# Kernel tuning notes

Measured on AMD Instinct MI355X. Metric: run time of the kernel, lower is better.

Reference implementation:

```python
import jax, jax.numpy as jnp
import numpy as np

N_NODES = 100000
N_EDGES = 1600000
NODE_FEAT_DIM = 140
NUM_OPCODES = 128
EMBED_DIM = 64
HIDDEN = 128
N_LAYERS = 4
LN_EPS = 1e-5


def _layer_norm(x, g, b):
    mu = jnp.mean(x, axis=-1, keepdims=True)
    var = jnp.mean(jnp.square(x - mu), axis=-1, keepdims=True)
    return (x - mu) * jax.lax.rsqrt(var + LN_EPS) * g + b


def setup_inputs() -> dict:
    key = jax.random.key(0)
    ks = jax.random.split(key, 16)
    node_feat = jax.random.normal(ks[0], (N_NODES, NODE_FEAT_DIM), dtype=jnp.float32)
    node_opcode = jax.random.randint(ks[1], (N_NODES,), 0, NUM_OPCODES)
    topo_depth = jax.random.uniform(ks[2], (N_NODES, 1), dtype=jnp.float32)
    edge_index = jax.random.randint(ks[3], (2, N_EDGES), 0, N_NODES)
    in_dim = NODE_FEAT_DIM + EMBED_DIM + 1  # 205
    s_in = 1.0 / np.sqrt(in_dim)
    s_h = 1.0 / np.sqrt(HIDDEN)
    embed = jax.random.normal(ks[4], (NUM_OPCODES, EMBED_DIM), dtype=jnp.float32)
    embed = embed.at[0].set(0.0)  # padding_idx=0
    W_in = jax.random.uniform(ks[5], (in_dim, HIDDEN), minval=-s_in, maxval=s_in, dtype=jnp.float32)
    b_in = jax.random.uniform(ks[6], (HIDDEN,), minval=-s_in, maxval=s_in, dtype=jnp.float32)
    ln0_g = jnp.ones((HIDDEN,), jnp.float32)
    ln0_b = jnp.zeros((HIDDEN,), jnp.float32)
    # SAGEConv per layer: lin_l (neighbors, with bias), lin_r (self, no bias)
    Wl = jax.random.uniform(ks[7], (N_LAYERS, HIDDEN, HIDDEN), minval=-s_h, maxval=s_h, dtype=jnp.float32)
    bl = jax.random.uniform(ks[8], (N_LAYERS, HIDDEN), minval=-s_h, maxval=s_h, dtype=jnp.float32)
    Wr = jax.random.uniform(ks[9], (N_LAYERS, HIDDEN, HIDDEN), minval=-s_h, maxval=s_h, dtype=jnp.float32)
    ln_g = jnp.ones((N_LAYERS, HIDDEN), jnp.float32)
    ln_b = jnp.zeros((N_LAYERS, HIDDEN), jnp.float32)
    return {"node_feat": node_feat, "topo_depth": topo_depth, "embed": embed,
            "W_in": W_in, "b_in": b_in, "ln0_g": ln0_g, "ln0_b": ln0_b,
            "Wl": Wl, "bl": bl, "Wr": Wr, "ln_g": ln_g, "ln_b": ln_b,
            "node_opcode": node_opcode, "edge_index": edge_index}


def reference(node_feat, topo_depth, embed, W_in, b_in, ln0_g, ln0_b,
              Wl, bl, Wr, ln_g, ln_b, node_opcode, edge_index):
    n = node_feat.shape[0]
    op = jnp.clip(node_opcode, 0, embed.shape[0] - 1)
    h = jnp.concatenate([node_feat, embed[op], topo_depth], axis=-1)  # (n, 205)
    # input_proj: Linear -> LayerNorm -> GELU (dropout = eval identity)
    h = jax.nn.gelu(_layer_norm(h @ W_in + b_in, ln0_g, ln0_b), approximate=False)
    src, tgt = edge_index[0], edge_index[1]
    deg = jax.ops.segment_sum(jnp.ones((src.shape[0],), h.dtype), tgt, num_segments=n)
    inv_deg = (1.0 / jnp.maximum(deg, 1.0))[:, None]
    for i in range(N_LAYERS):
        # mean-SAGE: aggregate source features onto targets
        agg = jax.ops.segment_sum(h[src], tgt, num_segments=n) * inv_deg
        out = agg @ Wl[i] + bl[i] + h @ Wr[i]
        h = _layer_norm(h + jax.nn.gelu(out, approximate=False), ln_g[i], ln_b[i])
    return h
```

## Files before the change

### kernel.cpp

```cpp
#include <hip/hip_runtime.h>
#include <cstdint>
#include <cstddef>

#define NN 100000
#define NE 1600000
#define FEAT 140
#define EMB 64
#define HID 128
#define LN_EPS 1e-5f
#define BK_SHIFT 9
#define NBUCK 196
#define MAXSEG 20480

typedef unsigned int uint;
typedef unsigned short ushort;
using short8 = __attribute__((ext_vector_type(8))) short;
using f32x4  = __attribute__((ext_vector_type(4))) float;

__device__ __forceinline__ float gelu_exact(float x) {
    return 0.5f * x * (1.0f + erff(x * 0.70710678118654752440f));
}

__device__ __forceinline__ ushort f2bf(float f) {
    uint u = __float_as_uint(f);
    uint r = (u + 0x7fff + ((u >> 16) & 1)) >> 16;
    return (ushort)r;
}

__device__ __forceinline__ float bf2f(ushort u) {
    return __uint_as_float(((uint)u) << 16);
}

__device__ __forceinline__ float bflo(uint u) {
    return __uint_as_float(u << 16);
}
__device__ __forceinline__ float bfhi(uint u) {
    return __uint_as_float(u & 0xffff0000u);
}

__global__ __launch_bounds__(256) void pack_weights_kernel(
    const float* __restrict__ W_in, const float* __restrict__ Wl,
    const float* __restrict__ Wr,
    ushort* __restrict__ winp, ushort* __restrict__ wcat)
{
    const int tid = blockIdx.x * 256 + threadIdx.x;
    const int NIN = 7 * 8 * 64;
    const int NL  = 8 * 8 * 64;
    if (tid < NIN) {
        const int kk = tid >> 9;
        const int c  = (tid >> 6) & 7;
        const int l  = tid & 63;
        const int kbase = kk * 32 + (l >> 4) * 8;
        const int col = c * 16 + (l & 15);
        short8 v;
        #pragma unroll
        for (int j = 0; j < 8; ++j) {
            const int k = kbase + j;
            v[j] = (k < 205) ? (short)f2bf(W_in[k * 128 + col]) : (short)0;
        }
        *(short8*)(winp + (size_t)tid * 8) = v;
    } else if (tid < NIN + 4 * NL) {
        const int t2 = tid - NIN;
        const int layer = t2 >> 12;
        const int r = t2 & (NL - 1);
        const int kk = r >> 9;
        const int c  = (r >> 6) & 7;
        const int l  = r & 63;
        const int kbase = kk * 32 + (l >> 4) * 8;
        const int col = c * 16 + (l & 15);
        short8 v;
        #pragma unroll
        for (int j = 0; j < 8; ++j) {
            const int k = kbase + j;
            const float x = (k < 128)
                ? Wl[(size_t)layer * 16384 + k * 128 + col]
                : Wr[(size_t)layer * 16384 + (k - 128) * 128 + col];
            v[j] = (short)f2bf(x);
        }
        *(short8*)(wcat + (size_t)t2 * 8) = v;
    }
}

__global__ __launch_bounds__(256) void input_proj_mfma(
    const float* __restrict__ nf, const float* __restrict__ topo,
    const float* __restrict__ embed, const int* __restrict__ opcode,
    const ushort* __restrict__ Wp, const float* __restrict__ b_in,
    const float* __restrict__ g0, const float* __restrict__ b0,
    ushort* __restrict__ hb_out)
{
    __shared__ ushort xs[64 * 232];
    const int t = threadIdx.x;
    const int node0 = blockIdx.x * 64;

    for (int idx = t; idx < 64 * 35; idx += 256) {
        const int row = idx / 35, c = idx - row * 35;
        const int node = min(node0 + row, NN - 1);
        const float4 v = ((const float4*)nf)[(size_t)node * 35 + c];
        ushort* p = &xs[row * 232 + c * 4];
        p[0] = f2bf(v.x); p[1] = f2bf(v.y); p[2] = f2bf(v.z); p[3] = f2bf(v.w);
    }
    for (int idx = t; idx < 64 * 16; idx += 256) {
        const int row = idx >> 4, c = idx & 15;
        const int node = min(node0 + row, NN - 1);
        int op = opcode[node];
        op = min(max(op, 0), 127);
        const float4 v = ((const float4*)embed)[op * 16 + c];
        ushort* p = &xs[row * 232 + 140 + c * 4];
        p[0] = f2bf(v.x); p[1] = f2bf(v.y); p[2] = f2bf(v.z); p[3] = f2bf(v.w);
    }
    if (t < 64) {
        const int node = min(node0 + t, NN - 1);
        xs[t * 232 + 204] = f2bf(topo[node]);
    }
    for (int idx = t; idx < 64 * 19; idx += 256) {
        const int row = idx / 19, c = 205 + (idx - row * 19);
        xs[row * 232 + c] = 0;
    }
    __syncthreads();

    const int w = t >> 6, l = t & 63;
    const int gq = l >> 4, li = l & 15;

    f32x4 acc[8];
    #pragma unroll
    for (int c = 0; c < 8; ++c) acc[c] = (f32x4){0.f, 0.f, 0.f, 0.f};

    const short8* Bp = (const short8*)Wp;
    for (int kk = 0; kk < 7; ++kk) {
        const short8 a = *(const short8*)&xs[(w * 16 + li) * 232 + kk * 32 + gq * 8];
        #pragma unroll
        for (int c = 0; c < 8; ++c) {
            const short8 b = Bp[(kk * 8 + c) * 64 + l];
            acc[c] = __builtin_amdgcn_mfma_f32_16x16x32_bf16(a, b, acc[c], 0, 0, 0);
        }
    }

    float bias[8], gam[8], bet[8];
    #pragma unroll
    for (int c = 0; c < 8; ++c) {
        bias[c] = b_in[c * 16 + li];
        gam[c]  = g0[c * 16 + li];
        bet[c]  = b0[c * 16 + li];
    }
    float s[4] = {0, 0, 0, 0}, q[4] = {0, 0, 0, 0};
    #pragma unroll
    for (int c = 0; c < 8; ++c)
        #pragma unroll
        for (int r = 0; r < 4; ++r) {
            const float u = acc[c][r] + bias[c];
            acc[c][r] = u;
            s[r] += u;
            q[r] += u * u;
        }
    #pragma unroll
    for (int off = 1; off < 16; off <<= 1)
        #pragma unroll
        for (int r = 0; r < 4; ++r) {
            s[r] += __shfl_xor(s[r], off);
            q[r] += __shfl_xor(q[r], off);
        }
    #pragma unroll
    for (int r = 0; r < 4; ++r) {
        const int node = node0 + w * 16 + gq * 4 + r;
        if (node >= NN) continue;
        const float mean = s[r] * (1.0f / HID);
        const float var  = q[r] * (1.0f / HID) - mean * mean;
        const float rstd = rsqrtf(var + LN_EPS);
        #pragma unroll
        for (int c = 0; c < 8; ++c) {
            const float y = gelu_exact((acc[c][r] - mean) * rstd * gam[c] + bet[c]);
            hb_out[(size_t)node * 128 + c * 16 + li] = f2bf(y);
        }
    }
}

__global__ __launch_bounds__(256) void hist_kernel(const int* __restrict__ tgt,
                                                   int* __restrict__ bhist) {
    __shared__ int lh[NBUCK];
    for (int i = threadIdx.x; i < NBUCK; i += 256) lh[i] = 0;
    __syncthreads();
    const int e0 = blockIdx.x * 8192;
    const int eend = min(e0 + 8192, NE);
    for (int e = e0 + threadIdx.x; e < eend; e += 256)
        atomicAdd(&lh[tgt[e] >> BK_SHIFT], 1);
    __syncthreads();
    for (int i = threadIdx.x; i < NBUCK; i += 256)
        if (lh[i]) atomicAdd(&bhist[i], lh[i]);
}

__global__ __launch_bounds__(256) void bucket_scan_kernel(const int* __restrict__ bhist,
                                                          int* __restrict__ bpos,
                                                          int* __restrict__ bcur) {
    __shared__ int s_[256];
    const int t = threadIdx.x;
    int v = (t < NBUCK) ? bhist[t] : 0;
    s_[t] = v;
    __syncthreads();
    for (int off = 1; off < 256; off <<= 1) {
        int u = (t >= off) ? s_[t - off] : 0;
        __syncthreads();
        s_[t] += u;
        __syncthreads();
    }
    if (t < NBUCK) { bpos[t] = s_[t] - v; bcur[t] = s_[t] - v; }
}

__global__ __launch_bounds__(256) void partition_kernel(const int* __restrict__ src,
                                                        const int* __restrict__ tgt,
                                                        int* __restrict__ bcur,
                                                        uint2* __restrict__ pairs) {
    __shared__ int lh[NBUCK];
    __shared__ int gbase[NBUCK];
    for (int i = threadIdx.x; i < NBUCK; i += 256) lh[i] = 0;
    __syncthreads();
    const int e0 = blockIdx.x * 2048;
    const int eend = min(e0 + 2048, NE);
    int myb[8], myr[8], mys[8], myt[8];
    int cnt = 0;
    for (int e = e0 + threadIdx.x; e < eend; e += 256) {
        const int tv = tgt[e];
        const int b = tv >> BK_SHIFT;
        myb[cnt] = b; myt[cnt] = tv; mys[cnt] = src[e];
        myr[cnt] = atomicAdd(&lh[b], 1);
        ++cnt;
    }
    __syncthreads();
    for (int i = threadIdx.x; i < NBUCK; i += 256)
        gbase[i] = lh[i] ? atomicAdd(&bcur[i], lh[i]) : 0;
    __syncthreads();
    for (int i = 0; i < cnt; ++i)
        pairs[gbase[myb[i]] + myr[i]] = make_uint2((uint)myt[i], (uint)mys[i]);
}

__global__ __launch_bounds__(256) void bucket_fill_kernel(const uint2* __restrict__ pairs,
                                                          const int* __restrict__ bpos,
                                                          const int* __restrict__ bhist,
                                                          int* __restrict__ offs,
                                                          float* __restrict__ inv_deg,
                                                          int* __restrict__ csr) {
    __shared__ int cnt[512];
    __shared__ int pref[512];
    __shared__ int ssum[256];
    __shared__ int stage[MAXSEG];
    const int t = threadIdx.x;
    const int b = blockIdx.x;
    const int n0 = b << BK_SHIFT;
    const int nn = min(512, NN - n0);
    const int p0 = bpos[b], pc = bhist[b];

    for (int i = t; i < 512; i += 256) cnt[i] = 0;
    __syncthreads();
    for (int i = t; i < pc; i += 256)
        atomicAdd(&cnt[(int)pairs[p0 + i].x - n0], 1);
    __syncthreads();
    const int a0 = cnt[2 * t], a1 = cnt[2 * t + 1];
    ssum[t] = a0 + a1;
    __syncthreads();
    for (int off = 1; off < 256; off <<= 1) {
        int u = (t >= off) ? ssum[t - off] : 0;
        __syncthreads();
        ssum[t] += u;
        __syncthreads();
    }
    const int ebase = ssum[t] - a0 - a1;
    pref[2 * t] = ebase;
    pref[2 * t + 1] = ebase + a0;
    __syncthreads();
    for (int i = t; i < nn; i += 256) {
        offs[n0 + i] = p0 + pref[i];
        inv_deg[n0 + i] = 1.0f / fmaxf((float)cnt[i], 1.0f);
    }
    if (b == NBUCK - 1 && t == 0) offs[NN] = NE;
    __syncthreads();
    for (int i = t; i < 512; i += 256) cnt[i] = 0;
    __syncthreads();
    if (pc <= MAXSEG) {
        for (int i = t; i < pc; i += 256) {
            const uint2 pr = pairs[p0 + i];
            const int ln = (int)pr.x - n0;
            const int p = atomicAdd(&cnt[ln], 1);
            stage[pref[ln] + p] = (int)pr.y;
        }
        __syncthreads();
        for (int i = t; i < pc; i += 256) csr[p0 + i] = stage[i];
    } else {
        for (int i = t; i < pc; i += 256) {
            const uint2 pr = pairs[p0 + i];
            const int ln = (int)pr.x - n0;
            const int p = atomicAdd(&cnt[ln], 1);
            csr[p0 + pref[ln] + p] = (int)pr.y;
        }
    }
}

__global__ __launch_bounds__(256) void gather_kernel(const ushort* __restrict__ hb,
                                                     const int* __restrict__ csr,
                                                     const int* __restrict__ offs,
                                                     const float* __restrict__ inv_deg,
                                                     ushort* __restrict__ aggb) {
    const int node = blockIdx.x * 4 + (threadIdx.x >> 6);
    const int lane = threadIdx.x & 63;
    if (node >= NN) return;
    const int beg = offs[node];
    const int end = offs[node + 1];
    const uint* hp = (const uint*)hb;
    float ax = 0.0f, ay = 0.0f;
    int j = beg;
    for (; j + 16 <= end; j += 16) {
        int ss[16];
        uint uu[16];
        #pragma unroll
        for (int i = 0; i < 16; ++i) ss[i] = csr[j + i];
        #pragma unroll
        for (int i = 0; i < 16; ++i) uu[i] = hp[(size_t)ss[i] * 64 + lane];
        float axp[4], ayp[4];
        #pragma unroll
        for (int p = 0; p < 4; ++p) {
            axp[p] = (bflo(uu[4 * p]) + bflo(uu[4 * p + 1])) + (bflo(uu[4 * p + 2]) + bflo(uu[4 * p + 3]));
            ayp[p] = (bfhi(uu[4 * p]) + bfhi(uu[4 * p + 1])) + (bfhi(uu[4 * p + 2]) + bfhi(uu[4 * p + 3]));
        }
        ax += (axp[0] + axp[1]) + (axp[2] + axp[3]);
        ay += (ayp[0] + ayp[1]) + (ayp[2] + ayp[3]);
    }
    for (; j + 4 <= end; j += 4) {
        int ss[4];
        uint uu[4];
        #pragma unroll
        for (int i = 0; i < 4; ++i) ss[i] = csr[j + i];
        #pragma unroll
        for (int i = 0; i < 4; ++i) uu[i] = hp[(size_t)ss[i] * 64 + lane];
        ax += (bflo(uu[0]) + bflo(uu[1])) + (bflo(uu[2]) + bflo(uu[3]));
        ay += (bfhi(uu[0]) + bfhi(uu[1])) + (bfhi(uu[2]) + bfhi(uu[3]));
    }
    for (; j < end; ++j) {
        uint u0 = hp[(size_t)csr[j] * 64 + lane];
        ax += bflo(u0);
        ay += bfhi(u0);
    }
    const float id = inv_deg[node];
    const uint lo = f2bf(ax * id);
    const uint hi = f2bf(ay * id);
    ((uint*)aggb)[(size_t)node * 64 + lane] = lo | (hi << 16);
}

__global__ __launch_bounds__(256) void layer_mfma(
    ushort* __restrict__ hb, const ushort* __restrict__ aggb,
    const ushort* __restrict__ Wp, const float* __restrict__ bl,
    const float* __restrict__ g, const float* __restrict__ b,
    float* __restrict__ hout, int write_f32)
{
    const int t = threadIdx.x;
    const int w = t >> 6, l = t & 63;
    const int gq = l >> 4, li = l & 15;
    const int node0 = blockIdx.x * 64;
    const int ar = min(node0 + w * 16 + li, NN - 1);

    f32x4 acc[8];
    #pragma unroll
    for (int c = 0; c < 8; ++c) acc[c] = (f32x4){0.f, 0.f, 0.f, 0.f};

    const short8* Bp = (const short8*)Wp;
    const short8* Ag = (const short8*)aggb;
    const short8* Hg = (const short8*)hb;
    #pragma unroll
    for (int kk = 0; kk < 8; ++kk) {
        const short8 a = (kk < 4) ? Ag[(size_t)ar * 16 + kk * 4 + gq]
                                  : Hg[(size_t)ar * 16 + (kk - 4) * 4 + gq];
        #pragma unroll
        for (int c = 0; c < 8; ++c) {
            const short8 bf = Bp[(kk * 8 + c) * 64 + l];
            acc[c] = __builtin_amdgcn_mfma_f32_16x16x32_bf16(a, bf, acc[c], 0, 0, 0);
        }
    }

    float bias[8], gam[8], bet[8];
    #pragma unroll
    for (int c = 0; c < 8; ++c) {
        bias[c] = bl[c * 16 + li];
        gam[c]  = g[c * 16 + li];
        bet[c]  = b[c * 16 + li];
    }
    float s[4] = {0, 0, 0, 0}, q[4] = {0, 0, 0, 0};
    #pragma unroll
    for (int r = 0; r < 4; ++r) {
        const int nd = min(node0 + w * 16 + gq * 4 + r, NN - 1);
        #pragma unroll
        for (int c = 0; c < 8; ++c) {
            const float hv = bf2f(hb[(size_t)nd * 128 + c * 16 + li]);
            const float tv = hv + gelu_exact(acc[c][r] + bias[c]);
            acc[c][r] = tv;
            s[r] += tv;
            q[r] += tv * tv;
        }
    }
    #pragma unroll
    for (int off = 1; off < 16; off <<= 1)
        #pragma unroll
        for (int r = 0; r < 4; ++r) {
            s[r] += __shfl_xor(s[r], off);
            q[r] += __shfl_xor(q[r], off);
        }
    #pragma unroll
    for (int r = 0; r < 4; ++r) {
        const int node = node0 + w * 16 + gq * 4 + r;
        if (node >= NN) continue;
        const float mean = s[r] * (1.0f / HID);
        const float var  = q[r] * (1.0f / HID) - mean * mean;
        const float rstd = rsqrtf(var + LN_EPS);
        #pragma unroll
        for (int c = 0; c < 8; ++c) {
            const float y = (acc[c][r] - mean) * rstd * gam[c] + bet[c];
            hb[(size_t)node * 128 + c * 16 + li] = f2bf(y);
            if (write_f32) hout[(size_t)node * 128 + c * 16 + li] = y;
        }
    }
}

extern "C" void kernel_launch(void* const* d_in, const int* in_sizes, int n_in,
                              void* d_out, int out_size, void* d_ws, size_t ws_size,
                              hipStream_t stream) {
    const float* node_feat = (const float*)d_in[0];
    const float* topo      = (const float*)d_in[1];
    const float* embed     = (const float*)d_in[2];
    const float* W_in      = (const float*)d_in[3];
    const float* b_in      = (const float*)d_in[4];
    const float* ln0_g     = (const float*)d_in[5];
    const float* ln0_b     = (const float*)d_in[6];
    const float* Wl        = (const float*)d_in[7];
    const float* bl        = (const float*)d_in[8];
    const float* Wr        = (const float*)d_in[9];
    const float* ln_g      = (const float*)d_in[10];
    const float* ln_b      = (const float*)d_in[11];
    const int*   opcode    = (const int*)d_in[12];
    const int*   edge      = (const int*)d_in[13];
    const int*   e_src = edge;
    const int*   e_tgt = edge + NE;

    float* h = (float*)d_out;

    char* w = (char*)d_ws;
    ushort* hb     = (ushort*)w;  w += (size_t)NN * HID * sizeof(ushort);
    ushort* aggb   = (ushort*)w;  w += (size_t)NN * HID * sizeof(ushort);
    float* inv_deg = (float*)w;   w += 400016;
    int*   offs    = (int*)w;     w += 400016;
    int*   bhist   = (int*)w;     w += 1024;
    int*   bpos    = (int*)w;     w += 1024;
    int*   bcur    = (int*)w;     w += 1024;
    int*   csr     = (int*)w;     w += (size_t)NE * sizeof(int);
    uint2* pairs   = (uint2*)w;   w += (size_t)NE * sizeof(uint2);
    ushort* winp   = (ushort*)w;  w += 7 * 8 * 64 * 8 * sizeof(ushort);
    ushort* wcat   = (ushort*)w;  w += 4 * 8 * 8 * 64 * 8 * sizeof(ushort);

    pack_weights_kernel<<<78, 256, 0, stream>>>(W_in, Wl, Wr, winp, wcat);

    input_proj_mfma<<<(NN + 63) / 64, 256, 0, stream>>>(
        node_feat, topo, embed, opcode, winp, b_in, ln0_g, ln0_b, hb);

    hipMemsetAsync(bhist, 0, NBUCK * sizeof(int), stream);
    hist_kernel<<<(NE + 8191) / 8192, 256, 0, stream>>>(e_tgt, bhist);
    bucket_scan_kernel<<<1, 256, 0, stream>>>(bhist, bpos, bcur);
    partition_kernel<<<(NE + 2047) / 2048, 256, 0, stream>>>(e_src, e_tgt, bcur, pairs);
    bucket_fill_kernel<<<NBUCK, 256, 0, stream>>>(pairs, bpos, bhist, offs, inv_deg, csr);

    for (int layer = 0; layer < 4; ++layer) {
        gather_kernel<<<NN / 4, 256, 0, stream>>>(hb, csr, offs, inv_deg, aggb);
        layer_mfma<<<(NN + 63) / 64, 256, 0, stream>>>(
            hb, aggb, wcat + (size_t)layer * 8 * 8 * 64 * 8,
            bl + (size_t)layer * HID,
            ln_g + (size_t)layer * HID, ln_b + (size_t)layer * HID,
            h, layer == 3 ? 1 : 0);
    }
}
```

Baseline: 566.2 us.

## Gather neighbor features from an fp8 copy of node activations

Adds an fp8 (e4m3) shadow copy of the hidden state, written alongside the bf16 copy by the input projection and each layer kernel. The gather kernel then reads 2 bytes per lane instead of 4, which halves the random-access traffic of neighbor aggregation. The fp8 buffer reuses the workspace of the edge-pair staging array, so input_proj is moved after CSR construction to avoid clobbering it. This adds extra byte-sized stores in the producer kernels and loses precision in the aggregated means, which risks tolerance failures.

```diff
diff --git a/kernel.cpp b/kernel.cpp
--- a/kernel.cpp
+++ b/kernel.cpp
@@ -14,8 +14,16 @@
 
 typedef unsigned int uint;
 typedef unsigned short ushort;
+typedef unsigned char uchar;
 using short8 = __attribute__((ext_vector_type(8))) short;
 using f32x4  = __attribute__((ext_vector_type(4))) float;
+using f32x2  = __attribute__((ext_vector_type(2))) float;
+
+#if defined(__has_builtin)
+#if __has_builtin(__builtin_amdgcn_cvt_pk_f32_fp8) && __has_builtin(__builtin_amdgcn_cvt_pk_fp8_f32)
+#define HAVE_FP8_CVT 1
+#endif
+#endif
 
 __device__ __forceinline__ float gelu_exact(float x) {
     return 0.5f * x * (1.0f + erff(x * 0.70710678118654752440f));
@@ -31,11 +39,34 @@
     return __uint_as_float(((uint)u) << 16);
 }
 
-__device__ __forceinline__ float bflo(uint u) {
-    return __uint_as_float(u << 16);
-}
-__device__ __forceinline__ float bfhi(uint u) {
-    return __uint_as_float(u & 0xffff0000u);
+__device__ __forceinline__ uchar f2fp8(float f) {
+#ifdef HAVE_FP8_CVT
+    return (uchar)(__builtin_amdgcn_cvt_pk_fp8_f32(f, f, 0, false) & 0xff);
+#else
+    uint u = __float_as_uint(f);
+    uint s = (u >> 24) & 0x80u;
+    uint t = u & 0x7fffffffu;
+    if (t >= 0x43E00000u) return (uchar)(s | 0x7Eu);
+    uint lsb = (t >> 20) & 1u;
+    t += 0x7FFFFu + lsb;
+    uint e = t >> 23;
+    if (e < 121u) return (uchar)s;
+    return (uchar)(s | ((e - 120u) << 3) | ((t >> 20) & 7u));
+#endif
+}
+
+__device__ __forceinline__ f32x2 fp8pair(uint u) {
+#ifdef HAVE_FP8_CVT
+    return __builtin_amdgcn_cvt_pk_f32_fp8((int)u, false);
+#else
+    uint b0 = u & 0xffu, b1 = (u >> 8) & 0xffu;
+    uint e0 = b0 & 0x7fu, e1 = b1 & 0x7fu;
+    uint s0 = (b0 & 0x80u) << 24, s1 = (b1 & 0x80u) << 24;
+    f32x2 r;
+    r[0] = __uint_as_float(e0 ? (s0 | ((e0 + 960u) << 20)) : s0);
+    r[1] = __uint_as_float(e1 ? (s1 | ((e1 + 960u) << 20)) : s1);
+    return r;
+#endif
 }
 
 __global__ __launch_bounds__(256) void pack_weights_kernel(
@@ -86,7 +117,7 @@
     const float* __restrict__ embed, const int* __restrict__ opcode,
     const ushort* __restrict__ Wp, const float* __restrict__ b_in,
     const float* __restrict__ g0, const float* __restrict__ b0,
-    ushort* __restrict__ hb_out)
+    ushort* __restrict__ hb_out, uchar* __restrict__ h8_out)
 {
     __shared__ ushort xs[64 * 232];
     const int t = threadIdx.x;
@@ -170,6 +201,7 @@
         for (int c = 0; c < 8; ++c) {
             const float y = gelu_exact((acc[c][r] - mean) * rstd * gam[c] + bet[c]);
             hb_out[(size_t)node * 128 + c * 16 + li] = f2bf(y);
+            h8_out[(size_t)node * 128 + c * 16 + li] = f2fp8(y);
         }
     }
 }
@@ -293,7 +325,7 @@
     }
 }
 
-__global__ __launch_bounds__(256) void gather_kernel(const ushort* __restrict__ hb,
+__global__ __launch_bounds__(256) void gather_kernel(const uchar* __restrict__ h8,
                                                      const int* __restrict__ csr,
                                                      const int* __restrict__ offs,
                                                      const float* __restrict__ inv_deg,
@@ -303,7 +335,7 @@
     if (node >= NN) return;
     const int beg = offs[node];
     const int end = offs[node + 1];
-    const uint* hp = (const uint*)hb;
+    const ushort* hp = (const ushort*)h8;
     float ax = 0.0f, ay = 0.0f;
     int j = beg;
     for (; j + 16 <= end; j += 16) {
@@ -316,8 +348,12 @@
         float axp[4], ayp[4];
         #pragma unroll
         for (int p = 0; p < 4; ++p) {
-            axp[p] = (bflo(uu[4 * p]) + bflo(uu[4 * p + 1])) + (bflo(uu[4 * p + 2]) + bflo(uu[4 * p + 3]));
-            ayp[p] = (bfhi(uu[4 * p]) + bfhi(uu[4 * p + 1])) + (bfhi(uu[4 * p + 2]) + bfhi(uu[4 * p + 3]));
+            f32x2 v0 = fp8pair(uu[4 * p + 0]);
+            f32x2 v1 = fp8pair(uu[4 * p + 1]);
+            f32x2 v2 = fp8pair(uu[4 * p + 2]);
+            f32x2 v3 = fp8pair(uu[4 * p + 3]);
+            axp[p] = (v0[0] + v1[0]) + (v2[0] + v3[0]);
+            ayp[p] = (v0[1] + v1[1]) + (v2[1] + v3[1]);
         }
         ax += (axp[0] + axp[1]) + (axp[2] + axp[3]);
         ay += (ayp[0] + ayp[1]) + (ayp[2] + ayp[3]);
@@ -329,13 +365,17 @@
         for (int i = 0; i < 4; ++i) ss[i] = csr[j + i];
         #pragma unroll
         for (int i = 0; i < 4; ++i) uu[i] = hp[(size_t)ss[i] * 64 + lane];
-        ax += (bflo(uu[0]) + bflo(uu[1])) + (bflo(uu[2]) + bflo(uu[3]));
-        ay += (bfhi(uu[0]) + bfhi(uu[1])) + (bfhi(uu[2]) + bfhi(uu[3]));
+        f32x2 v0 = fp8pair(uu[0]);
+        f32x2 v1 = fp8pair(uu[1]);
+        f32x2 v2 = fp8pair(uu[2]);
+        f32x2 v3 = fp8pair(uu[3]);
+        ax += (v0[0] + v1[0]) + (v2[0] + v3[0]);
+        ay += (v0[1] + v1[1]) + (v2[1] + v3[1]);
     }
     for (; j < end; ++j) {
-        uint u0 = hp[(size_t)csr[j] * 64 + lane];
-        ax += bflo(u0);
-        ay += bfhi(u0);
+        f32x2 v = fp8pair(hp[(size_t)csr[j] * 64 + lane]);
+        ax += v[0];
+        ay += v[1];
     }
     const float id = inv_deg[node];
     const uint lo = f2bf(ax * id);
@@ -344,7 +384,8 @@
 }
 
 __global__ __launch_bounds__(256) void layer_mfma(
-    ushort* __restrict__ hb, const ushort* __restrict__ aggb,
+    ushort* __restrict__ hb, uchar* __restrict__ h8,
+    const ushort* __restrict__ aggb,
     const ushort* __restrict__ Wp, const float* __restrict__ bl,
     const float* __restrict__ g, const float* __restrict__ b,
     float* __restrict__ hout, int write_f32)
@@ -411,6 +452,7 @@
         for (int c = 0; c < 8; ++c) {
             const float y = (acc[c][r] - mean) * rstd * gam[c] + bet[c];
             hb[(size_t)node * 128 + c * 16 + li] = f2bf(y);
+            h8[(size_t)node * 128 + c * 16 + li] = f2fp8(y);
             if (write_f32) hout[(size_t)node * 128 + c * 16 + li] = y;
         }
     }
@@ -447,14 +489,12 @@
     int*   bpos    = (int*)w;     w += 1024;
     int*   bcur    = (int*)w;     w += 1024;
     int*   csr     = (int*)w;     w += (size_t)NE * sizeof(int);
-    uint2* pairs   = (uint2*)w;   w += (size_t)NE * sizeof(uint2);
+    uint2* pairs   = (uint2*)w;
+    uchar* h8      = (uchar*)w;   w += (size_t)NE * sizeof(uint2);
     ushort* winp   = (ushort*)w;  w += 7 * 8 * 64 * 8 * sizeof(ushort);
     ushort* wcat   = (ushort*)w;  w += 4 * 8 * 8 * 64 * 8 * sizeof(ushort);
 
     pack_weights_kernel<<<78, 256, 0, stream>>>(W_in, Wl, Wr, winp, wcat);
-
-    input_proj_mfma<<<(NN + 63) / 64, 256, 0, stream>>>(
-        node_feat, topo, embed, opcode, winp, b_in, ln0_g, ln0_b, hb);
 
     hipMemsetAsync(bhist, 0, NBUCK * sizeof(int), stream);
     hist_kernel<<<(NE + 8191) / 8192, 256, 0, stream>>>(e_tgt, bhist);
@@ -462,10 +502,13 @@
     partition_kernel<<<(NE + 2047) / 2048, 256, 0, stream>>>(e_src, e_tgt, bcur, pairs);
     bucket_fill_kernel<<<NBUCK, 256, 0, stream>>>(pairs, bpos, bhist, offs, inv_deg, csr);
 
+    input_proj_mfma<<<(NN + 63) / 64, 256, 0, stream>>>(
+        node_feat, topo, embed, opcode, winp, b_in, ln0_g, ln0_b, hb, h8);
+
     for (int layer = 0; layer < 4; ++layer) {
-        gather_kernel<<<NN / 4, 256, 0, stream>>>(hb, csr, offs, inv_deg, aggb);
+        gather_kernel<<<NN / 4, 256, 0, stream>>>(h8, csr, offs, inv_deg, aggb);
         layer_mfma<<<(NN + 63) / 64, 256, 0, stream>>>(
-            hb, aggb, wcat + (size_t)layer * 8 * 8 * 64 * 8,
+            hb, h8, aggb, wcat + (size_t)layer * 8 * 8 * 64 * 8,
             bl + (size_t)layer * HID,
             ln_g + (size_t)layer * HID, ln_b + (size_t)layer * HID,
             h, layer == 3 ? 1 : 0);
```

Measured after the change: 556.9 us. No clear change (-1.6%).
